# Optimization experiments

Hardware: AMD Instinct MI355X
Metric: run time of the kernel (lower is better)

The kernel has to match this reference:

```python
import jax, jax.numpy as jnp
import numpy as np

NUM_HEADS = 8
HEAD_DIM = 64
SR = 2
LN_EPS = 1e-5


def _ln(x, g, b):
    # LayerNorm over last dim (torch nn.LayerNorm, eps=1e-5)
    m = jnp.mean(x, axis=-1, keepdims=True)
    v = jnp.var(x, axis=-1, keepdims=True)
    return (x - m) * jax.lax.rsqrt(v + LN_EPS) * g + b


def setup_inputs() -> dict:
    key = jax.random.key(0)
    ks = jax.random.split(key, 8)
    B, N, C = 8, 4096, 512
    Cc = 512                      # cross_dim
    inner = NUM_HEADS * HEAD_DIM  # 512
    w = lambda k, shp: jax.random.normal(k, shp, jnp.float32) * 0.02
    return {
        "x": jax.random.normal(ks[0], (B, N, C), jnp.float32),
        "y": jax.random.normal(ks[1], (B, 64 * 64, Cc), jnp.float32),
        "Wq": w(ks[2], (C, inner)),
        "Wkv": w(ks[3], (Cc, 2 * inner)),
        "Wproj": w(ks[4], (inner, C)),
        "bproj": jnp.zeros((C,), jnp.float32),
        "g_cross": jnp.ones((Cc,), jnp.float32),
        "b_cross": jnp.zeros((Cc,), jnp.float32),
        "sr_w": w(ks[5], (SR, SR, Cc, Cc)),   # HWIO conv kernel
        "sr_b": jnp.zeros((Cc,), jnp.float32),
        "g_sr": jnp.ones((Cc,), jnp.float32),
        "b_sr": jnp.zeros((Cc,), jnp.float32),
        "y_H": 64,
        "y_W": 64,
    }


def reference(x, y, Wq, Wkv, Wproj, bproj, g_cross, b_cross, sr_w, sr_b, g_sr, b_sr, y_H, y_W):
    B, N, C = x.shape
    h, d = NUM_HEADS, HEAD_DIM
    inner = h * d
    scale = d ** -0.5

    # q projection: [B, h, N, d]
    q = (x @ Wq).reshape(B, N, h, d).transpose(0, 2, 1, 3)

    # cross-attention norm on context
    y = _ln(y, g_cross, b_cross)
    Cc = y.shape[-1]

    # spatial reduction: conv(kernel=stride=SR) over [B, y_H, y_W, Cc]
    x_ = y.reshape(B, y_H, y_W, Cc)
    x_ = jax.lax.conv_general_dilated(
        x_, sr_w, window_strides=(SR, SR), padding='VALID',
        dimension_numbers=('NHWC', 'HWIO', 'NHWC')) + sr_b
    Nk = (y_H // SR) * (y_W // SR)
    x_ = _ln(x_.reshape(B, Nk, Cc), g_sr, b_sr)

    # kv projection: [2, B, h, Nk, d]
    kv = (x_ @ Wkv).reshape(B, Nk, 2, h, d).transpose(2, 0, 3, 1, 4)
    k, v = kv[0], kv[1]

    attn = jax.nn.softmax(jnp.einsum('bhnd,bhmd->bhnm', q, k) * scale, axis=-1)
    out = jnp.einsum('bhnm,bhmd->bhnd', attn, v)          # [B, h, N, d]
    out = out.transpose(0, 2, 1, 3).reshape(B, N, inner)  # [B, N, inner]
    return out @ Wproj + bproj
```

## Files before the change

### kernel.cpp

```cpp
#include <hip/hip_runtime.h>
#include <stdint.h>

typedef unsigned short u16;
typedef __attribute__((ext_vector_type(8))) short bf16x8;
typedef __attribute__((ext_vector_type(8))) unsigned short u16x8;
typedef __attribute__((ext_vector_type(4))) float f32x4;
typedef __attribute__((ext_vector_type(16))) float f32x16;
typedef __attribute__((ext_vector_type(4))) unsigned short u16x4;
typedef __attribute__((ext_vector_type(2))) unsigned int uint2v;

__device__ __forceinline__ u16 f2bf(float f) {
  unsigned u = __float_as_uint(f);
  u += 0x7fffu + ((u >> 16) & 1u);
  return (u16)(u >> 16);
}

__device__ __forceinline__ unsigned cvtpk(float lo, float hi) {
  unsigned r;
  asm("v_cvt_pk_bf16_f32 %0, %1, %2" : "=v"(r) : "v"(lo), "v"(hi));
  return r;
}

__device__ __forceinline__ void gload16(const u16* g, u16* l) {
  __builtin_amdgcn_global_load_lds(
      (const __attribute__((address_space(1))) unsigned int*)(uintptr_t)g,
      (__attribute__((address_space(3))) unsigned int*)(uintptr_t)l, 16, 0, 0);
}

#define WAITV(N) asm volatile("s_waitcnt vmcnt(" #N ")" ::: "memory")
#define BARRIER_FENCE()                  \
  __builtin_amdgcn_s_barrier();          \
  __builtin_amdgcn_sched_barrier(0)

__global__ __launch_bounds__(256) void transpose4_bf16(
    const float* __restrict__ W0, const float* __restrict__ W1,
    const float* __restrict__ W2, const float* __restrict__ W3,
    u16* __restrict__ T0, u16* __restrict__ T1, u16* __restrict__ T2,
    u16* __restrict__ T3) {
  __shared__ u16 lds[64][66];
  const float* W;
  u16* T;
  int R, C;
  switch (blockIdx.y) {
    case 0: W = W0; T = T0; R = 512; C = 512; break;
    case 1: W = W1; T = T1; R = 512; C = 1024; break;
    case 2: W = W2; T = T2; R = 512; C = 512; break;
    default: W = W3; T = T3; R = 2048; C = 512; break;
  }
  const int tilesC = C >> 6;
  const int nt = (R >> 6) * tilesC;
  const int tile = blockIdx.x;
  if (tile >= nt) return;
  const int tr = tile / tilesC, tc = tile - tr * tilesC;
  const int r0 = tr << 6, c0 = tc << 6;
  const int t = threadIdx.x;
  const int rr = t >> 2, cq = (t & 3) << 4;
  const float* src = W + (size_t)(r0 + rr) * C + c0 + cq;
  unsigned* ldsrow = (unsigned*)&lds[rr][cq];
#pragma unroll
  for (int j = 0; j < 4; j++) {
    f32x4 v = *(const f32x4*)(src + j * 4);
    ldsrow[j * 2] = cvtpk(v.x, v.y);
    ldsrow[j * 2 + 1] = cvtpk(v.z, v.w);
  }
  __syncthreads();
  const int oc = t >> 2, rq = (t & 3) << 4;
  u16x8 o0, o1;
#pragma unroll
  for (int j = 0; j < 8; j++) {
    o0[j] = lds[rq + j][oc];
    o1[j] = lds[rq + 8 + j][oc];
  }
  u16* dst = T + (size_t)(c0 + oc) * R + r0 + rq;
  *(u16x8*)dst = o0;
  *(u16x8*)(dst + 8) = o1;
}

__global__ __launch_bounds__(256) void cvt_bf16(const float* __restrict__ in,
                                                u16* __restrict__ out, int n4) {
  int i = blockIdx.x * 256 + threadIdx.x;
  if (i >= n4) return;
  f32x4 v = *(const f32x4*)(in + (size_t)i * 4);
  u16x4 o;
  o.x = f2bf(v.x); o.y = f2bf(v.y); o.z = f2bf(v.z); o.w = f2bf(v.w);
  *(u16x4*)(out + (size_t)i * 4) = o;
}

__global__ __launch_bounds__(256) void ln_y_im2col(
    const float* __restrict__ y, const float* __restrict__ g,
    const float* __restrict__ bb, u16* __restrict__ patches) {
  int row = blockIdx.x * 4 + (threadIdx.x >> 6);
  int l = threadIdx.x & 63;
  const float* yr = y + (size_t)row * 512;
  f32x4 v0 = *(const f32x4*)(yr + l * 4);
  f32x4 v1 = *(const f32x4*)(yr + 256 + l * 4);
  float s = v0.x + v0.y + v0.z + v0.w + v1.x + v1.y + v1.z + v1.w;
  float ss = v0.x * v0.x + v0.y * v0.y + v0.z * v0.z + v0.w * v0.w +
             v1.x * v1.x + v1.y * v1.y + v1.z * v1.z + v1.w * v1.w;
#pragma unroll
  for (int m = 1; m <= 32; m <<= 1) {
    s += __shfl_xor(s, m);
    ss += __shfl_xor(ss, m);
  }
  float mean = s * (1.0f / 512.0f);
  float inv = rsqrtf(ss * (1.0f / 512.0f) - mean * mean + 1e-5f);
  f32x4 g0 = *(const f32x4*)(g + l * 4), g1 = *(const f32x4*)(g + 256 + l * 4);
  f32x4 c0 = *(const f32x4*)(bb + l * 4), c1 = *(const f32x4*)(bb + 256 + l * 4);
  f32x4 o0 = (v0 - mean) * inv * g0 + c0;
  f32x4 o1 = (v1 - mean) * inv * g1 + c1;
  int b = row >> 12, n = row & 4095, r = n >> 6, cc = n & 63;
  u16* dst = patches +
             (size_t)((b << 10) + ((r >> 1) << 5) + (cc >> 1)) * 2048 +
             ((r & 1) * 2 + (cc & 1)) * 512;
  u16x4 w0, w1;
  w0.x = f2bf(o0.x); w0.y = f2bf(o0.y); w0.z = f2bf(o0.z); w0.w = f2bf(o0.w);
  w1.x = f2bf(o1.x); w1.y = f2bf(o1.y); w1.z = f2bf(o1.z); w1.w = f2bf(o1.w);
  *(u16x4*)(dst + l * 4) = w0;
  *(u16x4*)(dst + 256 + l * 4) = w1;
}

__global__ __launch_bounds__(256) void ln_rows(
    const float* __restrict__ in, const float* __restrict__ g,
    const float* __restrict__ bb, u16* __restrict__ out) {
  int row = blockIdx.x * 4 + (threadIdx.x >> 6);
  int l = threadIdx.x & 63;
  const float* xr = in + (size_t)row * 512;
  f32x4 v0 = *(const f32x4*)(xr + l * 4);
  f32x4 v1 = *(const f32x4*)(xr + 256 + l * 4);
  float s = v0.x + v0.y + v0.z + v0.w + v1.x + v1.y + v1.z + v1.w;
  float ss = v0.x * v0.x + v0.y * v0.y + v0.z * v0.z + v0.w * v0.w +
             v1.x * v1.x + v1.y * v1.y + v1.z * v1.z + v1.w * v1.w;
#pragma unroll
  for (int m = 1; m <= 32; m <<= 1) {
    s += __shfl_xor(s, m);
    ss += __shfl_xor(ss, m);
  }
  float mean = s * (1.0f / 512.0f);
  float inv = rsqrtf(ss * (1.0f / 512.0f) - mean * mean + 1e-5f);
  f32x4 g0 = *(const f32x4*)(g + l * 4), g1 = *(const f32x4*)(g + 256 + l * 4);
  f32x4 c0 = *(const f32x4*)(bb + l * 4), c1 = *(const f32x4*)(bb + 256 + l * 4);
  f32x4 o0 = (v0 - mean) * inv * g0 + c0;
  f32x4 o1 = (v1 - mean) * inv * g1 + c1;
  u16* dst = out + (size_t)row * 512;
  u16x4 w0, w1;
  w0.x = f2bf(o0.x); w0.y = f2bf(o0.y); w0.z = f2bf(o0.z); w0.w = f2bf(o0.w);
  w1.x = f2bf(o1.x); w1.y = f2bf(o1.y); w1.z = f2bf(o1.z); w1.w = f2bf(o1.w);
  *(u16x4*)(dst + l * 4) = w0;
  *(u16x4*)(dst + 256 + l * 4) = w1;
}

template <int EPI>
__global__ __launch_bounds__(256) void gemm_bt(
    const u16* __restrict__ A, const u16* __restrict__ BT, int M, int N, int K,
    float* __restrict__ OF, u16* __restrict__ OB, const float* __restrict__ bias,
    float scale, u16* __restrict__ KB, u16* __restrict__ VT) {
  __shared__ u16 As[3][128 * 32];
  __shared__ u16 Bs[3][128 * 32];
  const int tid = threadIdx.x;
  const int l = tid & 63, w = tid >> 6;
  const int brow = blockIdx.y * 128, bcol = blockIdx.x * 128;
  const int wr = w >> 1, wc = w & 1;
  const int lr = l & 15, lk = (l >> 4) * 8;
  const int srow = l >> 2, scol = (l & 3) * 8;
  const int r0s = w * 32 + srow, r1s = w * 32 + 16 + srow;
  const u16* Ap0 = &A[(size_t)(brow + r0s) * K + scol];
  const u16* Ap1 = &A[(size_t)(brow + r1s) * K + scol];
  const u16* Bp0 = &BT[(size_t)(bcol + r0s) * K + scol];
  const u16* Bp1 = &BT[(size_t)(bcol + r1s) * K + scol];
  const int lo0 = r0s * 32 + scol, lo1 = r1s * 32 + scol;
  f32x4 acc[4][4] = {};
  const int nt = K >> 5;
  gload16(Ap0, &As[0][lo0]);
  gload16(Ap1, &As[0][lo1]);
  gload16(Bp0, &Bs[0][lo0]);
  gload16(Bp1, &Bs[0][lo1]);
  gload16(Ap0 + 32, &As[1][lo0]);
  gload16(Ap1 + 32, &As[1][lo1]);
  gload16(Bp0 + 32, &Bs[1][lo0]);
  gload16(Bp1 + 32, &Bs[1][lo1]);
  int bufC = 0, bufS = 2;
  for (int t = 0; t < nt; ++t) {
    if (t + 1 < nt) WAITV(4);
    else WAITV(0);
    BARRIER_FENCE();
    if (t + 2 < nt) {
      int k0 = (t + 2) << 5;
      gload16(Ap0 + k0, &As[bufS][lo0]);
      gload16(Ap1 + k0, &As[bufS][lo1]);
      gload16(Bp0 + k0, &Bs[bufS][lo0]);
      gload16(Bp1 + k0, &Bs[bufS][lo1]);
    }
    bf16x8 af[4], bfr[4];
#pragma unroll
    for (int m = 0; m < 4; m++)
      af[m] = *(const bf16x8*)&As[bufC][(wr * 64 + m * 16 + lr) * 32 + lk];
#pragma unroll
    for (int n = 0; n < 4; n++)
      bfr[n] = *(const bf16x8*)&Bs[bufC][(wc * 64 + n * 16 + lr) * 32 + lk];
#pragma unroll
    for (int m = 0; m < 4; m++)
#pragma unroll
      for (int n = 0; n < 4; n++)
        acc[m][n] = __builtin_amdgcn_mfma_f32_16x16x32_bf16(af[m], bfr[n],
                                                            acc[m][n], 0, 0, 0);
    bufC = bufC == 2 ? 0 : bufC + 1;
    bufS = bufS == 2 ? 0 : bufS + 1;
  }
#pragma unroll
  for (int m = 0; m < 4; m++) {
    int r0 = brow + wr * 64 + m * 16 + (l >> 4) * 4;
#pragma unroll
    for (int n = 0; n < 4; n++) {
      int c = bcol + wc * 64 + n * 16 + lr;
#pragma unroll
      for (int j = 0; j < 4; j++) {
        float v = acc[m][n][j];
        int rrow = r0 + j;
        if (EPI == 0) {
          OF[(size_t)rrow * N + c] = v + bias[c];
        } else if (EPI == 2) {
          OB[(size_t)rrow * N + c] = f2bf(v * scale);
        } else {
          int b = rrow >> 10, nn = rrow & 1023;
          int dd = c & 63;
          if (c < 512) {
            int hh = c >> 6;
            KB[((size_t)((b * 8 + hh) * 1024 + nn)) * 64 + dd] = f2bf(v);
          } else {
            int hh = (c - 512) >> 6;
            VT[((size_t)((b * 8 + hh) * 64 + dd)) * 1024 + nn] = f2bf(v);
          }
        }
      }
    }
  }
}

__global__ __launch_bounds__(256) void gemm_bt64(
    const u16* __restrict__ A, const u16* __restrict__ BT, int M, int N, int K,
    float* __restrict__ OF, const float* __restrict__ bias) {
  __shared__ u16 As[3][64 * 32];
  __shared__ u16 Bs[3][128 * 32];
  const int tid = threadIdx.x;
  const int l = tid & 63, w = tid >> 6;
  const int brow = blockIdx.y * 64, bcol = blockIdx.x * 128;
  const int lr = l & 15, lk = (l >> 4) * 8;
  const int srow = tid >> 2, scol = (tid & 3) * 8;
  const u16* Ap = &A[(size_t)(brow + srow) * K + scol];
  const u16* Bp0 = &BT[(size_t)(bcol + srow) * K + scol];
  const u16* Bp1 = &BT[(size_t)(bcol + 64 + srow) * K + scol];
  const int loA = srow * 32 + scol;
  const int loB1 = (64 + srow) * 32 + scol;
  f32x4 acc[4][2] = {};
  const int nt = K >> 5;
  gload16(Ap, &As[0][loA]);
  gload16(Bp0, &Bs[0][loA]);
  gload16(Bp1, &Bs[0][loB1]);
  gload16(Ap + 32, &As[1][loA]);
  gload16(Bp0 + 32, &Bs[1][loA]);
  gload16(Bp1 + 32, &Bs[1][loB1]);
  int bufC = 0, bufS = 2;
  for (int t = 0; t < nt; ++t) {
    if (t + 1 < nt) WAITV(3);
    else WAITV(0);
    BARRIER_FENCE();
    if (t + 2 < nt) {
      int k0 = (t + 2) << 5;
      gload16(Ap + k0, &As[bufS][loA]);
      gload16(Bp0 + k0, &Bs[bufS][loA]);
      gload16(Bp1 + k0, &Bs[bufS][loB1]);
    }
    bf16x8 af[4], bfr[2];
#pragma unroll
    for (int m = 0; m < 4; m++)
      af[m] = *(const bf16x8*)&As[bufC][(m * 16 + lr) * 32 + lk];
#pragma unroll
    for (int n = 0; n < 2; n++)
      bfr[n] = *(const bf16x8*)&Bs[bufC][(w * 32 + n * 16 + lr) * 32 + lk];
#pragma unroll
    for (int m = 0; m < 4; m++)
#pragma unroll
      for (int n = 0; n < 2; n++)
        acc[m][n] = __builtin_amdgcn_mfma_f32_16x16x32_bf16(af[m], bfr[n],
                                                            acc[m][n], 0, 0, 0);
    bufC = bufC == 2 ? 0 : bufC + 1;
    bufS = bufS == 2 ? 0 : bufS + 1;
  }
#pragma unroll
  for (int m = 0; m < 4; m++) {
    int r0 = brow + m * 16 + (l >> 4) * 4;
#pragma unroll
    for (int n = 0; n < 2; n++) {
      int c = bcol + w * 32 + n * 16 + lr;
#pragma unroll
      for (int j = 0; j < 4; j++)
        OF[(size_t)(r0 + j) * N + c] = acc[m][n][j] + bias[c];
    }
  }
}

__global__ __launch_bounds__(256) void attn_fwd(
    const u16* __restrict__ q, const u16* __restrict__ kb,
    const u16* __restrict__ vt, u16* __restrict__ o) {
  __shared__ u16 Ks[3][32 * 64];
  __shared__ u16 Vs[3][64 * 32];
  const int idx = blockIdx.x;
  const int bh = ((idx >> 7) << 3) | (idx & 7);
  const int qb = (idx >> 3) & 15;
  const int b = bh >> 3, h = bh & 7;
  const int tid = threadIdx.x;
  const int w = tid >> 6, l = tid & 63;
  const int lq = l & 31, hi = l >> 5;
  const int qrowA = qb * 256 + w * 64 + lq;
  const int qrowB = qrowA + 32;
  const u16* qpA = q + (size_t)((b << 12) + qrowA) * 512 + h * 64 + hi * 8;
  const u16* qpB = q + (size_t)((b << 12) + qrowB) * 512 + h * 64 + hi * 8;
  bf16x8 qfA[4], qfB[4];
#pragma unroll
  for (int ds = 0; ds < 4; ds++) {
    qfA[ds] = *(const bf16x8*)(qpA + ds * 16);
    qfB[ds] = *(const bf16x8*)(qpB + ds * 16);
  }
  const short one = 0x3F80;
  const bf16x8 ones = {one, one, one, one, one, one, one, one};
  const u16* kp = kb + (size_t)bh * 65536;
  const u16* vtb = vt + (size_t)bh * 65536;
  const int krow = tid >> 3, kslot = tid & 7;
  const u16* ksrc = kp + krow * 64 + ((kslot ^ (krow & 7)) << 3);
  const int vrow = tid >> 2, vslot = tid & 3;
  const u16* vsrc = vtb + (size_t)vrow * 1024 + ((vslot ^ ((vrow >> 1) & 3)) << 3);
  const int kOff0 = lq * 64;
  const int vOff0 = lq * 32;
  const int vOff1 = (lq + 32) * 32;
  const int vmask = (lq >> 1) & 3;
  f32x16 oA0 = {}, oA1 = {}, oB0 = {}, oB1 = {};
  f32x16 smA = {}, smB = {};
  gload16(ksrc, &Ks[0][tid << 3]);
  gload16(vsrc, &Vs[0][tid << 3]);
  gload16(ksrc + 32 * 64, &Ks[1][tid << 3]);
  gload16(vsrc + 32, &Vs[1][tid << 3]);
  int bufC = 0, bufS = 2;
  for (int it = 0; it < 32; ++it) {
    if (it < 31) WAITV(2);
    else WAITV(0);
    BARRIER_FENCE();
    if (it + 2 < 32) {
      int kv2 = (it + 2) << 5;
      gload16(ksrc + kv2 * 64, &Ks[bufS][tid << 3]);
      gload16(vsrc + kv2, &Vs[bufS][tid << 3]);
    }
    const u16* Kc = Ks[bufC];
    const u16* Vc = Vs[bufC];
    bf16x8 kf[4];
#pragma unroll
    for (int ds = 0; ds < 4; ds++)
      kf[ds] = *(const bf16x8*)&Kc[kOff0 + ((((ds << 1) + hi) ^ (lq & 7)) << 3)];
    bf16x8 vf0[2], vf1[2];
#pragma unroll
    for (int t = 0; t < 2; t++) {
      int sw = (((t << 1) + hi) ^ vmask) << 3;
      vf0[t] = *(const bf16x8*)&Vc[vOff0 + sw];
      vf1[t] = *(const bf16x8*)&Vc[vOff1 + sw];
    }
    f32x16 stA = {}, stB = {};
#pragma unroll
    for (int ds = 0; ds < 4; ds++) {
      stA = __builtin_amdgcn_mfma_f32_32x32x16_bf16(kf[ds], qfA[ds], stA, 0, 0, 0);
      stB = __builtin_amdgcn_mfma_f32_32x32x16_bf16(kf[ds], qfB[ds], stB, 0, 0, 0);
    }
    bf16x8 pbA[2], pbB[2];
#pragma unroll
    for (int tile = 0; tile < 2; tile++) {
      f32x16& st = tile ? stB : stA;
      bf16x8* pb = tile ? pbB : pbA;
      float p[16];
#pragma unroll
      for (int r = 0; r < 16; r++) p[r] = __builtin_amdgcn_exp2f(st[r]);
#pragma unroll
      for (int t = 0; t < 2; t++) {
        unsigned c0 = cvtpk(p[8 * t + 0], p[8 * t + 1]);
        unsigned c1 = cvtpk(p[8 * t + 2], p[8 * t + 3]);
        unsigned c2 = cvtpk(p[8 * t + 4], p[8 * t + 5]);
        unsigned c3 = cvtpk(p[8 * t + 6], p[8 * t + 7]);
        uint2v r02 = __builtin_amdgcn_permlane32_swap(c0, c2, false, false);
        uint2v r13 = __builtin_amdgcn_permlane32_swap(c1, c3, false, false);
        union {
          unsigned u[4];
          bf16x8 v;
        } pk;
        pk.u[0] = r02.x;
        pk.u[1] = r13.x;
        pk.u[2] = r02.y;
        pk.u[3] = r13.y;
        pb[t] = pk.v;
      }
    }
#pragma unroll
    for (int t = 0; t < 2; t++) {
      oA0 = __builtin_amdgcn_mfma_f32_32x32x16_bf16(vf0[t], pbA[t], oA0, 0, 0, 0);
      oA1 = __builtin_amdgcn_mfma_f32_32x32x16_bf16(vf1[t], pbA[t], oA1, 0, 0, 0);
      smA = __builtin_amdgcn_mfma_f32_32x32x16_bf16(ones, pbA[t], smA, 0, 0, 0);
      oB0 = __builtin_amdgcn_mfma_f32_32x32x16_bf16(vf0[t], pbB[t], oB0, 0, 0, 0);
      oB1 = __builtin_amdgcn_mfma_f32_32x32x16_bf16(vf1[t], pbB[t], oB1, 0, 0, 0);
      smB = __builtin_amdgcn_mfma_f32_32x32x16_bf16(ones, pbB[t], smB, 0, 0, 0);
    }
    bufC = bufC == 2 ? 0 : bufC + 1;
    bufS = bufS == 2 ? 0 : bufS + 1;
  }
  const float invA = 1.0f / smA[0], invB = 1.0f / smB[0];
  u16* opA = o + (size_t)((b << 12) + qrowA) * 512 + h * 64;
  u16* opB = o + (size_t)((b << 12) + qrowB) * 512 + h * 64;
#pragma unroll
  for (int g = 0; g < 4; g++) {
    u16x4 a0, a1, b0, b1;
#pragma unroll
    for (int j = 0; j < 4; j++) {
      a0[j] = f2bf(oA0[g * 4 + j] * invA);
      a1[j] = f2bf(oA1[g * 4 + j] * invA);
      b0[j] = f2bf(oB0[g * 4 + j] * invB);
      b1[j] = f2bf(oB1[g * 4 + j] * invB);
    }
    *(u16x4*)(opA + 8 * g + 4 * hi) = a0;
    *(u16x4*)(opA + 32 + 8 * g + 4 * hi) = a1;
    *(u16x4*)(opB + 8 * g + 4 * hi) = b0;
    *(u16x4*)(opB + 32 + 8 * g + 4 * hi) = b1;
  }
}

extern "C" void kernel_launch(void* const* d_in, const int* in_sizes, int n_in,
                              void* d_out, int out_size, void* d_ws, size_t ws_size,
                              hipStream_t stream) {
  (void)in_sizes; (void)n_in; (void)out_size; (void)ws_size;
  const float* x = (const float*)d_in[0];
  const float* y = (const float*)d_in[1];
  const float* Wq = (const float*)d_in[2];
  const float* Wkv = (const float*)d_in[3];
  const float* Wproj = (const float*)d_in[4];
  const float* bproj = (const float*)d_in[5];
  const float* g_cross = (const float*)d_in[6];
  const float* b_cross = (const float*)d_in[7];
  const float* srw = (const float*)d_in[8];
  const float* sr_b = (const float*)d_in[9];
  const float* g_sr = (const float*)d_in[10];
  const float* b_sr = (const float*)d_in[11];
  float* out = (float*)d_out;

  u16* p = (u16*)d_ws;
  u16* WqT = p;    p += (size_t)512 * 512;
  u16* WkvT = p;   p += (size_t)1024 * 512;
  u16* WprojT = p; p += (size_t)512 * 512;
  u16* srwT = p;   p += (size_t)512 * 2048;
  u16* kbuf = p;   p += (size_t)8 * 8 * 1024 * 64;
  u16* vtbuf = p;  p += (size_t)8 * 8 * 1024 * 64;
  u16* xln = p;    p += (size_t)8192 * 512;
  u16* R1 = p;     p += (size_t)32768 * 512;
  u16* R2 = p;     p += (size_t)32768 * 512;
  u16* patches = R1;
  u16* xbf = R1;
  u16* attnb = R1;
  float* convout = (float*)R2;
  u16* qbuf = R2;

  transpose4_bf16<<<dim3(256, 4), 256, 0, stream>>>(Wq, Wkv, Wproj, srw,
                                                    WqT, WkvT, WprojT, srwT);
  ln_y_im2col<<<8192, 256, 0, stream>>>(y, g_cross, b_cross, patches);
  gemm_bt64<<<dim3(4, 128), 256, 0, stream>>>(patches, srwT, 8192, 512, 2048,
                                              convout, sr_b);
  ln_rows<<<2048, 256, 0, stream>>>(convout, g_sr, b_sr, xln);
  gemm_bt<1><<<dim3(8, 64), 256, 0, stream>>>(xln, WkvT, 8192, 1024, 512,
                                              nullptr, nullptr, nullptr, 1.0f,
                                              kbuf, vtbuf);
  cvt_bf16<<<16384, 256, 0, stream>>>(x, xbf, 32768 * 512 / 4);
  gemm_bt<2><<<dim3(4, 256), 256, 0, stream>>>(xbf, WqT, 32768, 512, 512,
                                               nullptr, qbuf, nullptr,
                                               0.125f * 1.44269504f,
                                               nullptr, nullptr);
  attn_fwd<<<dim3(1024), 256, 0, stream>>>(qbuf, kbuf, vtbuf, attnb);
  gemm_bt<0><<<dim3(4, 256), 256, 0, stream>>>(attnb, WprojT, 32768, 512, 512,
                                               out, nullptr, bproj, 1.0f,
                                               nullptr, nullptr);
}
```

Measured before the change: 250.3 us.

## Split-K the spatial-reduction conv GEMM and fuse partial sums into LayerNorm

The conv GEMM (8192x512, K=2048) now runs on the 128x128-tile gemm_bt with a two-way split over K (grid z=2), writing two fp32 partial outputs. The LayerNorm kernel is extended to add both partials plus the conv bias before normalizing, and the separate 64-row gemm_bt64 kernel is removed. The split is meant to improve MFMA tile efficiency and keep enough blocks in flight (512) with the larger tile. In exchange it writes and reads an extra fp32 partial buffer.

```diff
diff --git a/kernel.cpp b/kernel.cpp
--- a/kernel.cpp
+++ b/kernel.cpp
@@ -119,14 +119,22 @@
   *(u16x4*)(dst + 256 + l * 4) = w1;
 }
 
-__global__ __launch_bounds__(256) void ln_rows(
-    const float* __restrict__ in, const float* __restrict__ g,
+__global__ __launch_bounds__(256) void ln_rows2(
+    const float* __restrict__ inA, const float* __restrict__ inB,
+    const float* __restrict__ cb, const float* __restrict__ g,
     const float* __restrict__ bb, u16* __restrict__ out) {
   int row = blockIdx.x * 4 + (threadIdx.x >> 6);
   int l = threadIdx.x & 63;
-  const float* xr = in + (size_t)row * 512;
-  f32x4 v0 = *(const f32x4*)(xr + l * 4);
-  f32x4 v1 = *(const f32x4*)(xr + 256 + l * 4);
+  const float* ar = inA + (size_t)row * 512;
+  const float* br = inB + (size_t)row * 512;
+  f32x4 a0 = *(const f32x4*)(ar + l * 4);
+  f32x4 a1 = *(const f32x4*)(ar + 256 + l * 4);
+  f32x4 b0v = *(const f32x4*)(br + l * 4);
+  f32x4 b1v = *(const f32x4*)(br + 256 + l * 4);
+  f32x4 cb0 = *(const f32x4*)(cb + l * 4);
+  f32x4 cb1 = *(const f32x4*)(cb + 256 + l * 4);
+  f32x4 v0 = a0 + b0v + cb0;
+  f32x4 v1 = a1 + b1v + cb1;
   float s = v0.x + v0.y + v0.z + v0.w + v1.x + v1.y + v1.z + v1.w;
   float ss = v0.x * v0.x + v0.y * v0.y + v0.z * v0.z + v0.w * v0.w +
              v1.x * v1.x + v1.y * v1.y + v1.z * v1.z + v1.w * v1.w;
@@ -152,21 +160,23 @@
 template <int EPI>
 __global__ __launch_bounds__(256) void gemm_bt(
     const u16* __restrict__ A, const u16* __restrict__ BT, int M, int N, int K,
-    float* __restrict__ OF, u16* __restrict__ OB, const float* __restrict__ bias,
-    float scale, u16* __restrict__ KB, u16* __restrict__ VT) {
+    int ld, float* __restrict__ OF, u16* __restrict__ OB,
+    const float* __restrict__ bias, float scale, u16* __restrict__ KB,
+    u16* __restrict__ VT) {
   __shared__ u16 As[3][128 * 32];
   __shared__ u16 Bs[3][128 * 32];
   const int tid = threadIdx.x;
   const int l = tid & 63, w = tid >> 6;
   const int brow = blockIdx.y * 128, bcol = blockIdx.x * 128;
+  const int koff = blockIdx.z * K;
   const int wr = w >> 1, wc = w & 1;
   const int lr = l & 15, lk = (l >> 4) * 8;
   const int srow = l >> 2, scol = (l & 3) * 8;
   const int r0s = w * 32 + srow, r1s = w * 32 + 16 + srow;
-  const u16* Ap0 = &A[(size_t)(brow + r0s) * K + scol];
-  const u16* Ap1 = &A[(size_t)(brow + r1s) * K + scol];
-  const u16* Bp0 = &BT[(size_t)(bcol + r0s) * K + scol];
-  const u16* Bp1 = &BT[(size_t)(bcol + r1s) * K + scol];
+  const u16* Ap0 = &A[(size_t)(brow + r0s) * ld + koff + scol];
+  const u16* Ap1 = &A[(size_t)(brow + r1s) * ld + koff + scol];
+  const u16* Bp0 = &BT[(size_t)(bcol + r0s) * ld + koff + scol];
+  const u16* Bp1 = &BT[(size_t)(bcol + r1s) * ld + koff + scol];
   const int lo0 = r0s * 32 + scol, lo1 = r1s * 32 + scol;
   f32x4 acc[4][4] = {};
   const int nt = K >> 5;
@@ -206,6 +216,7 @@
     bufC = bufC == 2 ? 0 : bufC + 1;
     bufS = bufS == 2 ? 0 : bufS + 1;
   }
+  float* OFz = OF + (size_t)blockIdx.z * M * N;
 #pragma unroll
   for (int m = 0; m < 4; m++) {
     int r0 = brow + wr * 64 + m * 16 + (l >> 4) * 4;
@@ -220,6 +231,8 @@
           OF[(size_t)rrow * N + c] = v + bias[c];
         } else if (EPI == 2) {
           OB[(size_t)rrow * N + c] = f2bf(v * scale);
+        } else if (EPI == 4) {
+          OFz[(size_t)rrow * N + c] = v;
         } else {
           int b = rrow >> 10, nn = rrow & 1023;
           int dd = c & 63;
@@ -232,69 +245,6 @@
           }
         }
       }
-    }
-  }
-}
-
-__global__ __launch_bounds__(256) void gemm_bt64(
-    const u16* __restrict__ A, const u16* __restrict__ BT, int M, int N, int K,
-    float* __restrict__ OF, const float* __restrict__ bias) {
-  __shared__ u16 As[3][64 * 32];
-  __shared__ u16 Bs[3][128 * 32];
-  const int tid = threadIdx.x;
-  const int l = tid & 63, w = tid >> 6;
-  const int brow = blockIdx.y * 64, bcol = blockIdx.x * 128;
-  const int lr = l & 15, lk = (l >> 4) * 8;
-  const int srow = tid >> 2, scol = (tid & 3) * 8;
-  const u16* Ap = &A[(size_t)(brow + srow) * K + scol];
-  const u16* Bp0 = &BT[(size_t)(bcol + srow) * K + scol];
-  const u16* Bp1 = &BT[(size_t)(bcol + 64 + srow) * K + scol];
-  const int loA = srow * 32 + scol;
-  const int loB1 = (64 + srow) * 32 + scol;
-  f32x4 acc[4][2] = {};
-  const int nt = K >> 5;
-  gload16(Ap, &As[0][loA]);
-  gload16(Bp0, &Bs[0][loA]);
-  gload16(Bp1, &Bs[0][loB1]);
-  gload16(Ap + 32, &As[1][loA]);
-  gload16(Bp0 + 32, &Bs[1][loA]);
-  gload16(Bp1 + 32, &Bs[1][loB1]);
-  int bufC = 0, bufS = 2;
-  for (int t = 0; t < nt; ++t) {
-    if (t + 1 < nt) WAITV(3);
-    else WAITV(0);
-    BARRIER_FENCE();
-    if (t + 2 < nt) {
-      int k0 = (t + 2) << 5;
-      gload16(Ap + k0, &As[bufS][loA]);
-      gload16(Bp0 + k0, &Bs[bufS][loA]);
-      gload16(Bp1 + k0, &Bs[bufS][loB1]);
-    }
-    bf16x8 af[4], bfr[2];
-#pragma unroll
-    for (int m = 0; m < 4; m++)
-      af[m] = *(const bf16x8*)&As[bufC][(m * 16 + lr) * 32 + lk];
-#pragma unroll
-    for (int n = 0; n < 2; n++)
-      bfr[n] = *(const bf16x8*)&Bs[bufC][(w * 32 + n * 16 + lr) * 32 + lk];
-#pragma unroll
-    for (int m = 0; m < 4; m++)
-#pragma unroll
-      for (int n = 0; n < 2; n++)
-        acc[m][n] = __builtin_amdgcn_mfma_f32_16x16x32_bf16(af[m], bfr[n],
-                                                            acc[m][n], 0, 0, 0);
-    bufC = bufC == 2 ? 0 : bufC + 1;
-    bufS = bufS == 2 ? 0 : bufS + 1;
-  }
-#pragma unroll
-  for (int m = 0; m < 4; m++) {
-    int r0 = brow + m * 16 + (l >> 4) * 4;
-#pragma unroll
-    for (int n = 0; n < 2; n++) {
-      int c = bcol + w * 32 + n * 16 + lr;
-#pragma unroll
-      for (int j = 0; j < 4; j++)
-        OF[(size_t)(r0 + j) * N + c] = acc[m][n][j] + bias[c];
     }
   }
 }
@@ -458,25 +408,27 @@
   u16* patches = R1;
   u16* xbf = R1;
   u16* attnb = R1;
-  float* convout = (float*)R2;
+  float* convoutA = (float*)R2;
+  float* convoutB = convoutA + (size_t)8192 * 512;
   u16* qbuf = R2;
 
   transpose4_bf16<<<dim3(256, 4), 256, 0, stream>>>(Wq, Wkv, Wproj, srw,
                                                     WqT, WkvT, WprojT, srwT);
   ln_y_im2col<<<8192, 256, 0, stream>>>(y, g_cross, b_cross, patches);
-  gemm_bt64<<<dim3(4, 128), 256, 0, stream>>>(patches, srwT, 8192, 512, 2048,
-                                              convout, sr_b);
-  ln_rows<<<2048, 256, 0, stream>>>(convout, g_sr, b_sr, xln);
-  gemm_bt<1><<<dim3(8, 64), 256, 0, stream>>>(xln, WkvT, 8192, 1024, 512,
+  gemm_bt<4><<<dim3(4, 64, 2), 256, 0, stream>>>(
+      patches, srwT, 8192, 512, 1024, 2048, convoutA, nullptr, nullptr, 1.0f,
+      nullptr, nullptr);
+  ln_rows2<<<2048, 256, 0, stream>>>(convoutA, convoutB, sr_b, g_sr, b_sr, xln);
+  gemm_bt<1><<<dim3(8, 64), 256, 0, stream>>>(xln, WkvT, 8192, 1024, 512, 512,
                                               nullptr, nullptr, nullptr, 1.0f,
                                               kbuf, vtbuf);
   cvt_bf16<<<16384, 256, 0, stream>>>(x, xbf, 32768 * 512 / 4);
-  gemm_bt<2><<<dim3(4, 256), 256, 0, stream>>>(xbf, WqT, 32768, 512, 512,
+  gemm_bt<2><<<dim3(4, 256), 256, 0, stream>>>(xbf, WqT, 32768, 512, 512, 512,
                                                nullptr, qbuf, nullptr,
                                                0.125f * 1.44269504f,
                                                nullptr, nullptr);
   attn_fwd<<<dim3(1024), 256, 0, stream>>>(qbuf, kbuf, vtbuf, attnb);
   gemm_bt<0><<<dim3(4, 256), 256, 0, stream>>>(attnb, WprojT, 32768, 512, 512,
-                                               out, nullptr, bproj, 1.0f,
+                                               512, out, nullptr, bproj, 1.0f,
                                                nullptr, nullptr);
 }
```

Measured after the change: 245.5 us, median of 2. No clear change (-1.9%).
